# Performance work log

Hardware: AMD Instinct MI355X
Metric: run time of the kernel (lower is better)

Reference implementation:

```python
import jax, jax.numpy as jnp
import numpy as np

EPS_BN = 1e-5
EPS_W = 1e-8


def setup_inputs() -> dict:
    key = jax.random.key(0)
    ks = jax.random.split(key, 6)
    B, N, S, D1, D2 = 8, 8192, 2048, 128, 256
    Cin = D1 + D2  # 384
    return {
        "points_position": jax.random.normal(ks[0], (B, 3, N), jnp.float32),
        "sampled_points_position": jax.random.normal(ks[1], (B, 3, S), jnp.float32),
        "skip_points_feature": jax.random.normal(ks[2], (B, D1, N), jnp.float32),
        "sampled_points_feature": jax.random.normal(ks[3], (B, D2, S), jnp.float32),
        "W1": jax.random.normal(ks[4], (256, Cin), jnp.float32) * 0.05,
        "b1": jnp.zeros((256,), jnp.float32),
        "g1": jnp.ones((256,), jnp.float32),
        "beta1": jnp.zeros((256,), jnp.float32),
        "W2": jax.random.normal(ks[5], (128, 256), jnp.float32) * 0.05,
        "b2": jnp.zeros((128,), jnp.float32),
        "g2": jnp.ones((128,), jnp.float32),
        "beta2": jnp.zeros((128,), jnp.float32),
    }


def _bn_relu(x, g, b):
    # train-mode BatchNorm1d over (batch, points) per channel, x: [B,N,C]
    mean = jnp.mean(x, axis=(0, 1), keepdims=True)
    var = jnp.mean(jnp.square(x - mean), axis=(0, 1), keepdims=True)  # biased var
    return jax.nn.relu((x - mean) * jax.lax.rsqrt(var + EPS_BN) * g + b)


def reference(points_position, sampled_points_position, skip_points_feature,
              sampled_points_feature, W1, b1, g1, beta1, W2, b2, g2, beta2):
    pos = points_position.transpose(0, 2, 1)            # [B,N,3]
    spos = sampled_points_position.transpose(0, 2, 1)   # [B,S,3]
    sfeat = sampled_points_feature.transpose(0, 2, 1)   # [B,S,D2]

    # squared pairwise distance [B,N,S]
    d = (jnp.sum(pos * pos, axis=-1, keepdims=True)
         - 2.0 * jnp.einsum("bnc,bsc->bns", pos, spos)
         + jnp.sum(spos * spos, axis=-1)[:, None, :])

    # 3 nearest neighbors (smallest distances)
    neg_d3, idx = jax.lax.top_k(-d, 3)                  # [B,N,3]
    d3 = -neg_d3
    w = 1.0 / (d3 + EPS_W)
    w = w / jnp.sum(w, axis=-1, keepdims=True)          # [B,N,3]

    gathered = jax.vmap(lambda f, i: f[i])(sfeat, idx)  # [B,N,3,D2]
    interp = jnp.einsum("bnk,bnkd->bnd", w, gathered)   # [B,N,D2]

    feat = jnp.concatenate([skip_points_feature.transpose(0, 2, 1), interp], axis=-1)  # [B,N,D1+D2]

    h = _bn_relu(jnp.einsum("bnc,oc->bno", feat, W1) + b1, g1, beta1)  # [B,N,256]
    h = _bn_relu(jnp.einsum("bnc,oc->bno", h, W2) + b2, g2, beta2)     # [B,N,128]
    return h.transpose(0, 2, 1)                          # [B,128,N]
```

## Files before the change

kernel.cpp:

```cpp
#include <hip/hip_runtime.h>

constexpr int BATCH = 8;
constexpr int NPT   = 8192;
constexpr int NSMP  = 2048;
constexpr int D1C   = 128;
constexpr int D2C   = 256;
constexpr int CIN   = 384;
constexpr int C1    = 256;
constexpr int C2    = 128;
constexpr int BN_TOTAL = BATCH * NPT;

constexpr int BM = 128, BK = 32;
constexpr int NRB = BN_TOTAL / BM;

typedef __bf16 bf16x8 __attribute__((ext_vector_type(8)));
typedef short  s16x8  __attribute__((ext_vector_type(8)));
typedef float  f32x4  __attribute__((ext_vector_type(4)));
typedef unsigned short u16x4 __attribute__((ext_vector_type(4)));

__device__ __forceinline__ unsigned short f2bf(float x) {
  unsigned u = __builtin_bit_cast(unsigned, x);
  u += 0x7fffu + ((u >> 16) & 1u);
  return (unsigned short)(u >> 16);
}
__device__ __forceinline__ float bf2f(unsigned short h) {
  return __builtin_bit_cast(float, (unsigned)h << 16);
}

__device__ __forceinline__ void gld_lds16(const void* g, void* l) {
  __builtin_amdgcn_global_load_lds(
      (const __attribute__((address_space(1))) void*)g,
      (__attribute__((address_space(3))) void*)l, 16, 0, 0);
}

constexpr int PT_T = (NSMP / 32) * (D2C / 32) * BATCH;
constexpr int PT_S = (NPT / 32) * (D1C / 32) * BATCH;
constexpr int PT_M = (C1 * CIN + 255) / 256;

__global__ __launch_bounds__(256) void prep_all(
    const float* __restrict__ sfeat, float* __restrict__ sfeatT,
    const float* __restrict__ skip, unsigned short* __restrict__ featB,
    const float* __restrict__ spos, float* __restrict__ sposI,
    float4* __restrict__ qs4,
    const float* __restrict__ W1, unsigned short* __restrict__ W1h,
    const float* __restrict__ W2, unsigned short* __restrict__ W2h,
    float* __restrict__ stats) {
  __shared__ float tile[32][33];
  int bid = blockIdx.x, tid = threadIdx.x;
  int tx = tid & 31, ty = tid >> 5;
  if (bid < PT_T) {
    int z = bid >> 9;
    int r = bid & 511;
    int c0 = (r & 63) * 32;
    int r0 = (r >> 6) * 32;
    const float* inb = sfeat + (size_t)z * D2C * NSMP;
    float* outb = sfeatT + (size_t)z * NSMP * D2C;
#pragma unroll
    for (int i = 0; i < 32; i += 8)
      tile[ty + i][tx] = inb[(size_t)(r0 + ty + i) * NSMP + c0 + tx];
    __syncthreads();
#pragma unroll
    for (int i = 0; i < 32; i += 8)
      outb[(size_t)(c0 + ty + i) * D2C + r0 + tx] = tile[tx][ty + i];
  } else if (bid < PT_T + PT_S) {
    int id = bid - PT_T;
    int z = id >> 10;
    int r = id & 1023;
    int n0 = (r & 255) * 32;
    int d0 = (r >> 8) * 32;
#pragma unroll
    for (int i = 0; i < 32; i += 8)
      tile[ty + i][tx] = skip[((size_t)z * D1C + d0 + ty + i) * NPT + n0 + tx];
    __syncthreads();
#pragma unroll
    for (int i = 0; i < 32; i += 8) {
      int n = n0 + ty + i;
      featB[((size_t)z * NPT + n) * CIN + d0 + tx] = f2bf(tile[tx][ty + i]);
    }
  } else {
    int g = (bid - PT_T - PT_S) * 256 + tid;
    if (g < 768) stats[g] = 0.f;
    if (g < C1 * CIN) W1h[g] = f2bf(W1[g]);
    if (g < C2 * C1)  W2h[g] = f2bf(W2[g]);
    if (g < BATCH * NSMP) {
      int b = g >> 11, s = g & (NSMP - 1);
      const float* sp = spos + (size_t)b * 3 * NSMP;
      float x = sp[s], y = sp[NSMP + s], z = sp[2 * NSMP + s];
      sposI[(size_t)g * 3 + 0] = x;
      sposI[(size_t)g * 3 + 1] = y;
      sposI[(size_t)g * 3 + 2] = z;
      qs4[g] = make_float4(-2.f * x, -2.f * y, -2.f * z,
                           fmaf(x, x, fmaf(y, y, z * z)));
    }
  }
}

constexpr int KWAVES = 8;
constexpr int SEGK = NSMP / KWAVES;

__device__ __forceinline__ void ins_med3(float kf, float& k0, float& k1,
                                         float& k2, float& k3) {
  float o0 = k0, o1 = k1, o2 = k2;
  k0 = fminf(kf, o0);
  k1 = __builtin_amdgcn_fmed3f(kf, o0, o1);
  k2 = __builtin_amdgcn_fmed3f(kf, o1, o2);
  k3 = __builtin_amdgcn_fmed3f(kf, o2, k3);
}

__device__ __forceinline__ bool dless(double d, int i, double D, int I) {
  return d < D || (d == D && i < I);
}
__device__ __forceinline__ void dins3(double d, int i,
                                      double& b0, double& b1, double& b2,
                                      int& i0, int& i1, int& i2) {
  if (dless(d, i, b2, i2)) {
    if (dless(d, i, b1, i1)) {
      b2 = b1; i2 = i1;
      if (dless(d, i, b0, i0)) { b1 = b0; i1 = i0; b0 = d; i0 = i; }
      else                     { b1 = d; i1 = i; }
    } else { b2 = d; i2 = i; }
  }
}

__global__ __launch_bounds__(512, 2) void knn_all(
    const float* __restrict__ pos,
    const float4* __restrict__ qs4g,
    const float* __restrict__ sposI,
    const float* __restrict__ sfeatT,
    unsigned short* __restrict__ featB) {
  __shared__ __align__(16) unsigned char smem[NSMP * 16];
  float4* qs  = (float4*)smem;
  float*  mkf = (float*)smem;
#define MKF(w, sl, m, l) mkf[(w) * 1024 + ((sl) * 4 + (m)) * 64 + (l)]
  __shared__ int   il[256][3];
  __shared__ float wl[256][3];
  __shared__ int   fl[256];
  __shared__ int   fcnt;

  int tid = threadIdx.x;
  int wave = tid >> 6, lane = tid & 63;
  int blk = blockIdx.x;
  int b = blk & 7;
  int n0 = (blk >> 3) << 8;

  if (tid == 0) fcnt = 0;

  const float* pb = pos + (size_t)b * 3 * NPT;
  float px[4], py[4], pz[4], pp[4];
#pragma unroll
  for (int m = 0; m < 4; m++) {
    int n = n0 + (m << 6) + lane;
    px[m] = pb[n]; py[m] = pb[NPT + n]; pz[m] = pb[2 * NPT + n];
    pp[m] = fmaf(px[m], px[m], fmaf(py[m], py[m], pz[m] * pz[m]));
  }

  const float INF = __builtin_inff();
  float k0[4], k1[4], k2[4], k3[4];
#pragma unroll
  for (int m = 0; m < 4; m++) { k0[m] = INF; k1[m] = INF; k2[m] = INF; k3[m] = INF; }

  int s0 = wave * SEGK;
  const float4* qsrc = qs4g + (size_t)b * NSMP;
#pragma unroll
  for (int r = 0; r < 4; r++)
    gld_lds16(&qsrc[s0 + r * 64 + lane], &qs[s0 + r * 64]);
  __syncthreads();

#define KSTEP4(Q, SS)                                                        \
  {                                                                          \
    _Pragma("unroll")                                                        \
    for (int m_ = 0; m_ < 4; m_++) {                                         \
      float tt = (Q).w + pp[m_];       \
      float d_ = fmaf(px[m_], (Q).x,                                         \
                      fmaf(py[m_], (Q).y, fmaf(pz[m_], (Q).z, tt)));         \
      unsigned ki_ = (__builtin_bit_cast(unsigned, d_) & 0xFFFFF800u) |      \
                     (unsigned)(SS);                                         \
      ins_med3(__builtin_bit_cast(float, ki_), k0[m_], k1[m_], k2[m_], k3[m_]); \
    }                                                                        \
  }

  for (int t = 0; t < SEGK; t += 8) {
    float4 qv[8];
#pragma unroll
    for (int u = 0; u < 8; u++) qv[u] = qs[s0 + t + u];
#pragma unroll
    for (int u = 0; u < 8; u++) KSTEP4(qv[u], s0 + t + u)
  }
#undef KSTEP4

#pragma unroll
  for (int m = 0; m < 4; m++) {
    MKF(wave, 0, m, lane) = k0[m];
    MKF(wave, 1, m, lane) = k1[m];
    MKF(wave, 2, m, lane) = k2[m];
    MKF(wave, 3, m, lane) = k3[m];
  }
  __syncthreads();

  if (tid < 256) {
    int pm = tid >> 6, pl = tid & 63;
    float K0 = INF, K1 = INF, K2 = INF, K3 = INF;
#pragma unroll
    for (int w = 0; w < KWAVES; w++)
#pragma unroll
      for (int sl = 0; sl < 4; sl++)
        ins_med3(MKF(w, sl, pm, pl), K0, K1, K2, K3);

    int I0 = (int)(__builtin_bit_cast(unsigned, K0) & 0x7FFu);
    int I1 = (int)(__builtin_bit_cast(unsigned, K1) & 0x7FFu);
    int I2 = (int)(__builtin_bit_cast(unsigned, K2) & 0x7FFu);
    float d2m = __builtin_bit_cast(float, __builtin_bit_cast(unsigned, K2) & 0xFFFFF800u);
    float d3m = __builtin_bit_cast(float, __builtin_bit_cast(unsigned, K3) & 0xFFFFF800u);
    bool flag = (d3m - d2m) < 2e-3f * fmaxf(d3m, 0.f) + 1e-5f;
    if (flag) {
      int slot = atomicAdd(&fcnt, 1);
      fl[slot] = tid;
    }
    int n = n0 + tid;
    const float* q = sposI + (size_t)b * 3 * NSMP;
    double pxd = (double)pb[n], pyd = (double)pb[NPT + n], pzd = (double)pb[2 * NPT + n];
    double dd[3]; int II[3] = {I0, I1, I2};
#pragma unroll
    for (int k = 0; k < 3; k++) {
      double dx = pxd - (double)q[3 * II[k]];
      double dy = pyd - (double)q[3 * II[k] + 1];
      double dz = pzd - (double)q[3 * II[k] + 2];
      dd[k] = dx * dx + dy * dy + dz * dz;
    }
    double w0 = 1.0 / (dd[0] + 1e-8);
    double w1 = 1.0 / (dd[1] + 1e-8);
    double w2 = 1.0 / (dd[2] + 1e-8);
    double inv = 1.0 / (w0 + w1 + w2);
    il[tid][0] = I0; il[tid][1] = I1; il[tid][2] = I2;
    wl[tid][0] = (float)(w0 * inv);
    wl[tid][1] = (float)(w1 * inv);
    wl[tid][2] = (float)(w2 * inv);
  }
  __syncthreads();

  int fc = fcnt;
  for (int t = wave; t < fc; t += KWAVES) {
    int P = fl[t];
    int n = n0 + P;
    double pxd = (double)pb[n], pyd = (double)pb[NPT + n], pzd = (double)pb[2 * NPT + n];
    const float* q = sposI + (size_t)b * 3 * NSMP;
    double b0 = 1e300, b1 = 1e300, b2 = 1e300;
    int i0 = 0x7FFFFFFF, i1 = 0x7FFFFFFF, i2 = 0x7FFFFFFF;
    for (int s = lane; s < NSMP; s += 64) {
      double dx = pxd - (double)q[3 * s];
      double dy = pyd - (double)q[3 * s + 1];
      double dz = pzd - (double)q[3 * s + 2];
      double d = dx * dx + dy * dy + dz * dz;
      dins3(d, s, b0, b1, b2, i0, i1, i2);
    }
#pragma unroll
    for (int m = 1; m < 64; m <<= 1) {
      double o0 = __shfl_xor(b0, m, 64), o1 = __shfl_xor(b1, m, 64), o2 = __shfl_xor(b2, m, 64);
      int    j0 = __shfl_xor(i0, m, 64), j1 = __shfl_xor(i1, m, 64), j2 = __shfl_xor(i2, m, 64);
      dins3(o0, j0, b0, b1, b2, i0, i1, i2);
      dins3(o1, j1, b0, b1, b2, i0, i1, i2);
      dins3(o2, j2, b0, b1, b2, i0, i1, i2);
    }
    if (lane == 0) {
      double w0 = 1.0 / (b0 + 1e-8);
      double w1 = 1.0 / (b1 + 1e-8);
      double w2 = 1.0 / (b2 + 1e-8);
      double inv = 1.0 / (w0 + w1 + w2);
      il[P][0] = i0; il[P][1] = i1; il[P][2] = i2;
      wl[P][0] = (float)(w0 * inv);
      wl[P][1] = (float)(w1 * inv);
      wl[P][2] = (float)(w2 * inv);
    }
  }
  __syncthreads();

  const float* base = sfeatT + (size_t)b * NSMP * D2C;
  for (int i = 0; i < 32; i++) {
    int P = (wave << 5) + i;
    int i0 = il[P][0], i1 = il[P][1], i2 = il[P][2];
    float w0 = wl[P][0], w1 = wl[P][1], w2 = wl[P][2];
    float4 v0 = *(const float4*)&base[(size_t)i0 * D2C + (lane << 2)];
    float4 v1 = *(const float4*)&base[(size_t)i1 * D2C + (lane << 2)];
    float4 v2 = *(const float4*)&base[(size_t)i2 * D2C + (lane << 2)];
    u16x4 o;
    o[0] = f2bf(w0 * v0.x + w1 * v1.x + w2 * v2.x);
    o[1] = f2bf(w0 * v0.y + w1 * v1.y + w2 * v2.y);
    o[2] = f2bf(w0 * v0.z + w1 * v1.z + w2 * v2.z);
    o[3] = f2bf(w0 * v0.w + w1 * v1.w + w2 * v2.w);
    *(u16x4*)&featB[((size_t)b * NPT + n0 + P) * CIN + D1C + (lane << 2)] = o;
  }
#undef MKF
}

__global__ __launch_bounds__(256) void gemm1_mw(
    const unsigned short* __restrict__ featB,
    const unsigned short* __restrict__ W1h,
    const float* __restrict__ bias,
    unsigned short* __restrict__ Y1,
    float* __restrict__ sum1,
    float* __restrict__ sumsq1) {
  __shared__ __align__(16) unsigned short As[BM * BK];
  __shared__ __align__(16) unsigned short Bs[BM * BK];
  int tid = threadIdx.x;
  int lane = tid & 63, w = tid >> 6;
  int wr = w >> 1, wc = w & 1;
  int m16 = lane & 15, quad = lane >> 4;
  int cb = blockIdx.x, rb = blockIdx.y;
  int row0 = rb * BM, col0 = cb * BM;
  int srow = lane >> 2, scol8 = (lane & 3) * 8;

  f32x4 acc[4][4];
#pragma unroll
  for (int j = 0; j < 4; j++) {
    float bj = bias[col0 + wc * 64 + j * 16 + m16];
#pragma unroll
    for (int i = 0; i < 4; i++) acc[i][j] = f32x4{bj, bj, bj, bj};
  }

  for (int k0 = 0; k0 < CIN; k0 += BK) {
#pragma unroll
    for (int kq = 0; kq < 2; kq++) {
      int ar = 32 * w + 16 * kq + srow;
      int lb = __builtin_amdgcn_readfirstlane((32 * w + 16 * kq) * BK);
      gld_lds16(&featB[(size_t)(row0 + ar) * CIN + k0 + scol8], &As[lb]);
      gld_lds16(&W1h[(size_t)(col0 + ar) * CIN + k0 + scol8], &Bs[lb]);
    }
    __syncthreads();

    bf16x8 a[4], bb[4];
#pragma unroll
    for (int i = 0; i < 4; i++)
      a[i] = __builtin_bit_cast(bf16x8,
          *(const s16x8*)&As[(wr * 64 + i * 16 + m16) * BK + quad * 8]);
#pragma unroll
    for (int j = 0; j < 4; j++)
      bb[j] = __builtin_bit_cast(bf16x8,
          *(const s16x8*)&Bs[(wc * 64 + j * 16 + m16) * BK + quad * 8]);
#pragma unroll
    for (int i = 0; i < 4; i++)
#pragma unroll
      for (int j = 0; j < 4; j++)
        acc[i][j] = __builtin_amdgcn_mfma_f32_16x16x32_bf16(a[i], bb[j], acc[i][j], 0, 0, 0);
    __syncthreads();
  }

#pragma unroll
  for (int j = 0; j < 4; j++) {
    int col = col0 + wc * 64 + j * 16 + m16;
    float s = 0.f, q = 0.f;
#pragma unroll
    for (int i = 0; i < 4; i++)
#pragma unroll
      for (int r = 0; r < 4; r++) {
        float v = acc[i][j][r];
        Y1[(size_t)(row0 + wr * 64 + i * 16 + quad * 4 + r) * C1 + col] = f2bf(v);
        s += v; q = fmaf(v, v, q);
      }
    s += __shfl_xor(s, 16, 64); s += __shfl_xor(s, 32, 64);
    q += __shfl_xor(q, 16, 64); q += __shfl_xor(q, 32, 64);
    if (quad == 0) {
      atomicAdd(&sum1[col], s);
      atomicAdd(&sumsq1[col], q);
    }
  }
}

__global__ __launch_bounds__(256) void gemm2_mw(
    const unsigned short* __restrict__ Y1,
    const float* __restrict__ g1, const float* __restrict__ beta1,
    const float* __restrict__ sum1, const float* __restrict__ sumsq1,
    const unsigned short* __restrict__ W2h,
    const float* __restrict__ bias,
    unsigned short* __restrict__ Y2,
    float* __restrict__ sum2, float* __restrict__ sumsq2) {
  __shared__ __align__(16) unsigned short As[BM * BK];
  __shared__ __align__(16) unsigned short Bs[BM * BK];
  __shared__ float scs[C1], shs[C1];
  int tid = threadIdx.x;
  int lane = tid & 63, w = tid >> 6;
  int wr = w >> 1, wc = w & 1;
  int m16 = lane & 15, quad = lane >> 4;
  int rb = blockIdx.x;
  int row0 = rb * BM, col0 = 0;
  int srow = lane >> 2, scol8 = (lane & 3) * 8;

  {
    const float invBN = 1.0f / (float)BN_TOTAL;
    float mean = sum1[tid] * invBN;
    float var = sumsq1[tid] * invBN - mean * mean;
    float sc = g1[tid] / sqrtf(var + 1e-5f);
    scs[tid] = sc;
    shs[tid] = beta1[tid] - mean * sc;
  }

  f32x4 acc[4][4];
#pragma unroll
  for (int j = 0; j < 4; j++) {
    float bj = bias[col0 + wc * 64 + j * 16 + m16];
#pragma unroll
    for (int i = 0; i < 4; i++) acc[i][j] = f32x4{bj, bj, bj, bj};
  }
  __syncthreads();

  for (int k0 = 0; k0 < C1; k0 += BK) {
#pragma unroll
    for (int kq = 0; kq < 2; kq++) {
      int ar = 32 * w + 16 * kq + srow;
      int lb = __builtin_amdgcn_readfirstlane((32 * w + 16 * kq) * BK);
      gld_lds16(&W2h[(size_t)(col0 + ar) * C1 + k0 + scol8], &Bs[lb]);
      s16x8 v = *(const s16x8*)&Y1[(size_t)(row0 + ar) * C1 + k0 + scol8];
      unsigned short ov[8];
#pragma unroll
      for (int e = 0; e < 8; e++) {
        float x = bf2f((unsigned short)v[e]);
        float y = fmaxf(fmaf(x, scs[k0 + scol8 + e], shs[k0 + scol8 + e]), 0.f);
        ov[e] = f2bf(y);
      }
      *(s16x8*)&As[ar * BK + scol8] = *(const s16x8*)ov;
    }
    __syncthreads();

    bf16x8 a[4], bb[4];
#pragma unroll
    for (int i = 0; i < 4; i++)
      a[i] = __builtin_bit_cast(bf16x8,
          *(const s16x8*)&As[(wr * 64 + i * 16 + m16) * BK + quad * 8]);
#pragma unroll
    for (int j = 0; j < 4; j++)
      bb[j] = __builtin_bit_cast(bf16x8,
          *(const s16x8*)&Bs[(wc * 64 + j * 16 + m16) * BK + quad * 8]);
#pragma unroll
    for (int i = 0; i < 4; i++)
#pragma unroll
      for (int j = 0; j < 4; j++)
        acc[i][j] = __builtin_amdgcn_mfma_f32_16x16x32_bf16(a[i], bb[j], acc[i][j], 0, 0, 0);
    __syncthreads();
  }

#pragma unroll
  for (int j = 0; j < 4; j++) {
    int col = col0 + wc * 64 + j * 16 + m16;
    float s = 0.f, q = 0.f;
#pragma unroll
    for (int i = 0; i < 4; i++)
#pragma unroll
      for (int r = 0; r < 4; r++) {
        float v = acc[i][j][r];
        Y2[(size_t)(row0 + wr * 64 + i * 16 + quad * 4 + r) * C2 + col] = f2bf(v);
        s += v; q = fmaf(v, v, q);
      }
    s += __shfl_xor(s, 16, 64); s += __shfl_xor(s, 32, 64);
    q += __shfl_xor(q, 16, 64); q += __shfl_xor(q, 32, 64);
    if (quad == 0) {
      atomicAdd(&sum2[col], s);
      atomicAdd(&sumsq2[col], q);
    }
  }
}

__global__ void final_kernel(const unsigned short* __restrict__ Y2,
                             const float* __restrict__ sum2,
                             const float* __restrict__ sumsq2,
                             const float* __restrict__ g2,
                             const float* __restrict__ beta2,
                             float* __restrict__ out) {
  __shared__ float tile[32][33];
  int b = blockIdx.z;
  int n0 = blockIdx.x * 32;
  int c0 = blockIdx.y * 32;
  int tx = threadIdx.x, ty = threadIdx.y;
  int c = c0 + tx;
  const float invBN = 1.0f / (float)BN_TOTAL;
  float mean = sum2[c] * invBN;
  float var = sumsq2[c] * invBN - mean * mean;
  float sc = g2[c] / sqrtf(var + 1e-5f);
  float sh = beta2[c] - mean * sc;
#pragma unroll
  for (int i = 0; i < 32; i += 8) {
    int n = n0 + ty + i;
    float v = bf2f(Y2[((size_t)b * NPT + n) * C2 + c0 + tx]);
    tile[ty + i][tx] = fmaxf(fmaf(v, sc, sh), 0.f);
  }
  __syncthreads();
#pragma unroll
  for (int i = 0; i < 32; i += 8) {
    int cc = c0 + ty + i;
    out[((size_t)b * C2 + cc) * NPT + n0 + tx] = tile[tx][ty + i];
  }
}

extern "C" void kernel_launch(void* const* d_in, const int* in_sizes, int n_in,
                              void* d_out, int out_size, void* d_ws, size_t ws_size,
                              hipStream_t stream) {
  (void)in_sizes; (void)n_in; (void)out_size; (void)ws_size;
  const float* pos   = (const float*)d_in[0];
  const float* spos  = (const float*)d_in[1];
  const float* skip  = (const float*)d_in[2];
  const float* sfeat = (const float*)d_in[3];
  const float* W1    = (const float*)d_in[4];
  const float* b1    = (const float*)d_in[5];
  const float* g1    = (const float*)d_in[6];
  const float* beta1 = (const float*)d_in[7];
  const float* W2    = (const float*)d_in[8];
  const float* b2    = (const float*)d_in[9];
  const float* g2    = (const float*)d_in[10];
  const float* beta2 = (const float*)d_in[11];
  float* out = (float*)d_out;

  float* ws = (float*)d_ws;
  size_t off = 0;
  float* sfeatT  = ws + off; off += (size_t)BATCH * NSMP * D2C;
  unsigned short* featB = (unsigned short*)(ws + off); off += (size_t)BN_TOTAL * CIN / 2;
  unsigned short* Y1    = (unsigned short*)(ws + off); off += (size_t)BN_TOTAL * C1 / 2;
  unsigned short* Y2    = (unsigned short*)(ws + off); off += (size_t)BN_TOTAL * C2 / 2;
  unsigned short* W1h   = (unsigned short*)(ws + off); off += (size_t)C1 * CIN / 2;
  unsigned short* W2h   = (unsigned short*)(ws + off); off += (size_t)C2 * C1 / 2;
  float* sposI   = ws + off; off += (size_t)BATCH * NSMP * 3;
  float4* qs4    = (float4*)(ws + off); off += (size_t)BATCH * NSMP * 4;
  float* stats   = ws + off; off += 1024;
  float* sum1   = stats;
  float* sumsq1 = stats + 256;
  float* sum2   = stats + 512;
  float* sumsq2 = stats + 640;

  prep_all<<<PT_T + PT_S + PT_M, 256, 0, stream>>>(
      sfeat, sfeatT, skip, featB, spos, sposI, qs4, W1, W1h, W2, W2h, stats);

  knn_all<<<BN_TOTAL / 256, 512, 0, stream>>>(pos, qs4, sposI, sfeatT, featB);

  gemm1_mw<<<dim3(C1 / BM, NRB), 256, 0, stream>>>(
      featB, W1h, b1, Y1, sum1, sumsq1);

  gemm2_mw<<<NRB, 256, 0, stream>>>(
      Y1, g1, beta1, sum1, sumsq1, W2h, b2, Y2, sum2, sumsq2);

  final_kernel<<<dim3(NPT / 32, C2 / 32, BATCH), dim3(32, 8), 0, stream>>>(
      Y2, sum2, sumsq2, g2, beta2, out);
}
```

Baseline: 287.7 us.

## Split KNN into scan kernel and separate merge/refine/gather kernel

Splits the fused knn_all kernel in two. knn_scan writes per-wave top-4 candidate keys to a global buffer. knn_post then merges them, does the double-precision refinement for ambiguous points and gathers the interpolated features, using smaller 64-point blocks. This aims to spread the serial merge, the refine tail and the gather across many more blocks instead of leaving most of the 512-thread block idle. The cost is an extra launch and a 32×BN_TOTAL float round trip through global memory, about 8 MB each way.

```diff
diff --git a/kernel.cpp b/kernel.cpp
--- a/kernel.cpp
+++ b/kernel.cpp
@@ -107,43 +107,17 @@
   k3 = __builtin_amdgcn_fmed3f(kf, o2, k3);
 }
 
-__device__ __forceinline__ bool dless(double d, int i, double D, int I) {
-  return d < D || (d == D && i < I);
-}
-__device__ __forceinline__ void dins3(double d, int i,
-                                      double& b0, double& b1, double& b2,
-                                      int& i0, int& i1, int& i2) {
-  if (dless(d, i, b2, i2)) {
-    if (dless(d, i, b1, i1)) {
-      b2 = b1; i2 = i1;
-      if (dless(d, i, b0, i0)) { b1 = b0; i1 = i0; b0 = d; i0 = i; }
-      else                     { b1 = d; i1 = i; }
-    } else { b2 = d; i2 = i; }
-  }
-}
-
-__global__ __launch_bounds__(512, 2) void knn_all(
+__global__ __launch_bounds__(512, 2) void knn_scan(
     const float* __restrict__ pos,
     const float4* __restrict__ qs4g,
-    const float* __restrict__ sposI,
-    const float* __restrict__ sfeatT,
-    unsigned short* __restrict__ featB) {
-  __shared__ __align__(16) unsigned char smem[NSMP * 16];
-  float4* qs  = (float4*)smem;
-  float*  mkf = (float*)smem;
-#define MKF(w, sl, m, l) mkf[(w) * 1024 + ((sl) * 4 + (m)) * 64 + (l)]
-  __shared__ int   il[256][3];
-  __shared__ float wl[256][3];
-  __shared__ int   fl[256];
-  __shared__ int   fcnt;
+    float* __restrict__ mkG) {
+  __shared__ __align__(16) float4 qs[NSMP];
 
   int tid = threadIdx.x;
   int wave = tid >> 6, lane = tid & 63;
   int blk = blockIdx.x;
   int b = blk & 7;
   int n0 = (blk >> 3) << 8;
-
-  if (tid == 0) fcnt = 0;
 
   const float* pb = pos + (size_t)b * 3 * NPT;
   float px[4], py[4], pz[4], pp[4];
@@ -188,23 +162,63 @@
   }
 #undef KSTEP4
 
+  size_t gbase = (size_t)b * NPT + n0 + lane;
 #pragma unroll
   for (int m = 0; m < 4; m++) {
-    MKF(wave, 0, m, lane) = k0[m];
-    MKF(wave, 1, m, lane) = k1[m];
-    MKF(wave, 2, m, lane) = k2[m];
-    MKF(wave, 3, m, lane) = k3[m];
-  }
+    size_t gp = gbase + (m << 6);
+    mkG[(size_t)(wave * 4 + 0) * BN_TOTAL + gp] = k0[m];
+    mkG[(size_t)(wave * 4 + 1) * BN_TOTAL + gp] = k1[m];
+    mkG[(size_t)(wave * 4 + 2) * BN_TOTAL + gp] = k2[m];
+    mkG[(size_t)(wave * 4 + 3) * BN_TOTAL + gp] = k3[m];
+  }
+}
+
+__device__ __forceinline__ bool dless(double d, int i, double D, int I) {
+  return d < D || (d == D && i < I);
+}
+__device__ __forceinline__ void dins3(double d, int i,
+                                      double& b0, double& b1, double& b2,
+                                      int& i0, int& i1, int& i2) {
+  if (dless(d, i, b2, i2)) {
+    if (dless(d, i, b1, i1)) {
+      b2 = b1; i2 = i1;
+      if (dless(d, i, b0, i0)) { b1 = b0; i1 = i0; b0 = d; i0 = i; }
+      else                     { b1 = d; i1 = i; }
+    } else { b2 = d; i2 = i; }
+  }
+}
+
+constexpr int PPB_P = 64;
+
+__global__ __launch_bounds__(256) void knn_post(
+    const float* __restrict__ pos,
+    const float* __restrict__ sposI,
+    const float* __restrict__ mkG,
+    const float* __restrict__ sfeatT,
+    unsigned short* __restrict__ featB) {
+  __shared__ int   il[PPB_P][3];
+  __shared__ float wl[PPB_P][3];
+  __shared__ int   fl[PPB_P];
+  __shared__ int   fcnt;
+
+  int tid = threadIdx.x;
+  int wave = tid >> 6, lane = tid & 63;
+  int blk = blockIdx.x;
+  int b = blk & 7;
+  int n0 = (blk >> 3) * PPB_P;
+
+  if (tid == 0) fcnt = 0;
   __syncthreads();
 
-  if (tid < 256) {
-    int pm = tid >> 6, pl = tid & 63;
+  const float* pb = pos + (size_t)b * 3 * NPT;
+  const float INF = __builtin_inff();
+
+  if (tid < PPB_P) {
+    size_t gp = (size_t)b * NPT + n0 + tid;
     float K0 = INF, K1 = INF, K2 = INF, K3 = INF;
 #pragma unroll
-    for (int w = 0; w < KWAVES; w++)
-#pragma unroll
-      for (int sl = 0; sl < 4; sl++)
-        ins_med3(MKF(w, sl, pm, pl), K0, K1, K2, K3);
+    for (int pl = 0; pl < 32; pl++)
+      ins_med3(mkG[(size_t)pl * BN_TOTAL + gp], K0, K1, K2, K3);
 
     int I0 = (int)(__builtin_bit_cast(unsigned, K0) & 0x7FFu);
     int I1 = (int)(__builtin_bit_cast(unsigned, K1) & 0x7FFu);
@@ -239,7 +253,7 @@
   __syncthreads();
 
   int fc = fcnt;
-  for (int t = wave; t < fc; t += KWAVES) {
+  for (int t = wave; t < fc; t += 4) {
     int P = fl[t];
     int n = n0 + P;
     double pxd = (double)pb[n], pyd = (double)pb[NPT + n], pzd = (double)pb[2 * NPT + n];
@@ -275,8 +289,8 @@
   __syncthreads();
 
   const float* base = sfeatT + (size_t)b * NSMP * D2C;
-  for (int i = 0; i < 32; i++) {
-    int P = (wave << 5) + i;
+  for (int i = 0; i < 16; i++) {
+    int P = (wave << 4) + i;
     int i0 = il[P][0], i1 = il[P][1], i2 = il[P][2];
     float w0 = wl[P][0], w1 = wl[P][1], w2 = wl[P][2];
     float4 v0 = *(const float4*)&base[(size_t)i0 * D2C + (lane << 2)];
@@ -289,7 +303,6 @@
     o[3] = f2bf(w0 * v0.w + w1 * v1.w + w2 * v2.w);
     *(u16x4*)&featB[((size_t)b * NPT + n0 + P) * CIN + D1C + (lane << 2)] = o;
   }
-#undef MKF
 }
 
 __global__ __launch_bounds__(256) void gemm1_mw(
@@ -517,6 +530,7 @@
   unsigned short* W2h   = (unsigned short*)(ws + off); off += (size_t)C2 * C1 / 2;
   float* sposI   = ws + off; off += (size_t)BATCH * NSMP * 3;
   float4* qs4    = (float4*)(ws + off); off += (size_t)BATCH * NSMP * 4;
+  float* mkG     = ws + off; off += (size_t)32 * BN_TOTAL;
   float* stats   = ws + off; off += 1024;
   float* sum1   = stats;
   float* sumsq1 = stats + 256;
@@ -526,7 +540,9 @@
   prep_all<<<PT_T + PT_S + PT_M, 256, 0, stream>>>(
       sfeat, sfeatT, skip, featB, spos, sposI, qs4, W1, W1h, W2, W2h, stats);
 
-  knn_all<<<BN_TOTAL / 256, 512, 0, stream>>>(pos, qs4, sposI, sfeatT, featB);
+  knn_scan<<<BN_TOTAL / 256, 512, 0, stream>>>(pos, qs4, mkG);
+
+  knn_post<<<BN_TOTAL / PPB_P, 256, 0, stream>>>(pos, sposI, mkG, sfeatT, featB);
 
   gemm1_mw<<<dim3(C1 / BM, NRB), 256, 0, stream>>>(
       featB, W1h, b1, Y1, sum1, sumsq1);
```

Result: slower. 303.5 us (+5.5%).
